# Performance work log

Hardware: AMD Instinct MI355X
Metric: run time of the kernel (lower is better)

## Reference

```python
import jax, jax.numpy as jnp
import numpy as np


def setup_inputs() -> dict:
    key = jax.random.key(0)
    k1, k2 = jax.random.split(key)
    B, Q, LD, D = 64, 32, 4096, 128
    query_embeds = jax.random.normal(k1, (B, Q, D), dtype=jnp.float32)
    doc_embeds = jax.random.normal(k2, (B, LD, D), dtype=jnp.float32)
    return {"query_embeds": query_embeds, "doc_embeds": doc_embeds}


def reference(query_embeds, doc_embeds):
    # ColBERT MaxSim (similarity_metric='maxsim'):
    # torch: (q.unsqueeze(2) * d.unsqueeze(1)).sum(-1).max(dim=-1).values.sum(-1)
    # Efficient equivalent: batched GEMM then max over doc tokens, sum over query tokens.
    # scores: [B, Q, Ld]
    scores = jnp.einsum('bqd,bld->bql', query_embeds, doc_embeds)
    # max over doc tokens (Ld), sum over query tokens (Q) -> [B]
    return jnp.max(scores, axis=-1).sum(axis=-1)
```

## Files before the change

### kernel.cpp

```cpp
#include <hip/hip_runtime.h>
#include <hip/hip_bf16.h>

typedef __attribute__((ext_vector_type(8))) short bf16x8;
typedef __attribute__((ext_vector_type(4))) float f32x4;

static constexpr int Bb = 64;
static constexpr int Qq = 32;
static constexpr int LD = 4096;
static constexpr int Dd = 128;
static constexpr int SPLITS = 8;
static constexpr int CHUNK = LD / SPLITS;
static constexpr int NWAVE = 4;
static constexpr int TPW = CHUNK / NWAVE;
static constexpr int LTILES = TPW / 16;

__device__ __forceinline__ short f2bf(float f) {
  __hip_bfloat16 h = __float2bfloat16(f);
  return *reinterpret_cast<short*>(&h);
}

__device__ __forceinline__ bf16x8 pack8(const float* __restrict__ src) {
  float4 f0 = *reinterpret_cast<const float4*>(src);
  float4 f1 = *reinterpret_cast<const float4*>(src + 4);
  bf16x8 v;
  v[0] = f2bf(f0.x); v[1] = f2bf(f0.y); v[2] = f2bf(f0.z); v[3] = f2bf(f0.w);
  v[4] = f2bf(f1.x); v[5] = f2bf(f1.y); v[6] = f2bf(f1.z); v[7] = f2bf(f1.w);
  return v;
}

__global__ __launch_bounds__(256) void maxsim_stage1(
    const float* __restrict__ qe, const float* __restrict__ de,
    float* __restrict__ pmax) {
  const int blk  = blockIdx.x;
  const int b    = blk / SPLITS;
  const int s    = blk % SPLITS;
  const int wave = threadIdx.x >> 6;
  const int lane = threadIdx.x & 63;
  const int lcol = lane & 15;
  const int lgrp = lane >> 4;

  const float* __restrict__ qb = qe + (size_t)b * Qq * Dd;
  const float* __restrict__ db = de + (size_t)b * LD * Dd;

  bf16x8 afrag[2][4];
#pragma unroll
  for (int mt = 0; mt < 2; ++mt)
#pragma unroll
    for (int kb = 0; kb < 4; ++kb)
      afrag[mt][kb] = pack8(qb + (size_t)(mt * 16 + lcol) * Dd + kb * 32 + lgrp * 8);

  float mx0[4], mx1[4];
#pragma unroll
  for (int i = 0; i < 4; ++i) { mx0[i] = -3.4e38f; mx1[i] = -3.4e38f; }

  const int tok0 = s * CHUNK + wave * TPW;
  for (int lt = 0; lt < LTILES; ++lt) {
    const float* __restrict__ trow = db + (size_t)(tok0 + lt * 16 + lcol) * Dd;
    f32x4 acc0 = {0.f, 0.f, 0.f, 0.f};
    f32x4 acc1 = {0.f, 0.f, 0.f, 0.f};
#pragma unroll
    for (int kb = 0; kb < 4; ++kb) {
      bf16x8 bfrag = pack8(trow + kb * 32 + lgrp * 8);
      acc0 = __builtin_amdgcn_mfma_f32_16x16x32_bf16(afrag[0][kb], bfrag, acc0, 0, 0, 0);
      acc1 = __builtin_amdgcn_mfma_f32_16x16x32_bf16(afrag[1][kb], bfrag, acc1, 0, 0, 0);
    }
#pragma unroll
    for (int i = 0; i < 4; ++i) {
      mx0[i] = fmaxf(mx0[i], acc0[i]);
      mx1[i] = fmaxf(mx1[i], acc1[i]);
    }
  }

#pragma unroll
  for (int off = 1; off < 16; off <<= 1) {
#pragma unroll
    for (int i = 0; i < 4; ++i) {
      mx0[i] = fmaxf(mx0[i], __shfl_xor(mx0[i], off));
      mx1[i] = fmaxf(mx1[i], __shfl_xor(mx1[i], off));
    }
  }

  __shared__ float smax[NWAVE][Qq];
  if (lcol == 0) {
#pragma unroll
    for (int i = 0; i < 4; ++i) {
      smax[wave][lgrp * 4 + i]      = mx0[i];
      smax[wave][16 + lgrp * 4 + i] = mx1[i];
    }
  }
  __syncthreads();
  if (threadIdx.x < Qq) {
    const int qi = threadIdx.x;
    float m = fmaxf(fmaxf(smax[0][qi], smax[1][qi]),
                    fmaxf(smax[2][qi], smax[3][qi]));
    pmax[((size_t)b * SPLITS + s) * Qq + qi] = m;
  }
}

__global__ __launch_bounds__(64) void maxsim_stage2(
    const float* __restrict__ pmax, float* __restrict__ out) {
  const int b = blockIdx.x;
  const int lane = threadIdx.x;
  float v = 0.f;
  if (lane < Qq) {
    float m = -3.4e38f;
#pragma unroll
    for (int s = 0; s < SPLITS; ++s)
      m = fmaxf(m, pmax[((size_t)b * SPLITS + s) * Qq + lane]);
    v = m;
  }
#pragma unroll
  for (int off = 1; off < 64; off <<= 1) v += __shfl_xor(v, off);
  if (lane == 0) out[b] = v;
}

extern "C" void kernel_launch(void* const* d_in, const int* in_sizes, int n_in,
                              void* d_out, int out_size, void* d_ws, size_t ws_size,
                              hipStream_t stream) {
  const float* qe = (const float*)d_in[0];
  const float* de = (const float*)d_in[1];
  float* out  = (float*)d_out;
  float* pmax = (float*)d_ws;

  maxsim_stage1<<<Bb * SPLITS, 256, 0, stream>>>(qe, de, pmax);
  maxsim_stage2<<<Bb, 64, 0, stream>>>(pmax, out);
}
```

Baseline: 32.01 us.

## Split query tiles across waves, double splits, and remap block order

Each wave now handles a single 16-row query tile instead of both, so the two tile waves read the same doc tokens. Splits double to 16 and blocks grow to 512 threads, with a full unroll of the token loop to put more loads in flight. Block indices are permuted so consecutive blocks land on different batch regions, which may spread traffic across XCDs. Doc data is now loaded and converted to bf16 by two waves instead of one, which doubles global reads (mostly L2 hits) and conversion work.

```diff
diff --git a/kernel.cpp b/kernel.cpp
--- a/kernel.cpp
+++ b/kernel.cpp
@@ -8,10 +8,11 @@
 static constexpr int Qq = 32;
 static constexpr int LD = 4096;
 static constexpr int Dd = 128;
-static constexpr int SPLITS = 8;
+static constexpr int SPLITS = 16;
 static constexpr int CHUNK = LD / SPLITS;
-static constexpr int NWAVE = 4;
-static constexpr int TPW = CHUNK / NWAVE;
+static constexpr int NWAVE = 8;
+static constexpr int NRANGE = NWAVE / 2;
+static constexpr int TPW = CHUNK / NRANGE;
 static constexpr int LTILES = TPW / 16;
 
 __device__ __forceinline__ short f2bf(float f) {
@@ -19,22 +20,22 @@
   return *reinterpret_cast<short*>(&h);
 }
 
-__device__ __forceinline__ bf16x8 pack8(const float* __restrict__ src) {
-  float4 f0 = *reinterpret_cast<const float4*>(src);
-  float4 f1 = *reinterpret_cast<const float4*>(src + 4);
+__device__ __forceinline__ bf16x8 cvt8(float4 a, float4 b) {
   bf16x8 v;
-  v[0] = f2bf(f0.x); v[1] = f2bf(f0.y); v[2] = f2bf(f0.z); v[3] = f2bf(f0.w);
-  v[4] = f2bf(f1.x); v[5] = f2bf(f1.y); v[6] = f2bf(f1.z); v[7] = f2bf(f1.w);
+  v[0] = f2bf(a.x); v[1] = f2bf(a.y); v[2] = f2bf(a.z); v[3] = f2bf(a.w);
+  v[4] = f2bf(b.x); v[5] = f2bf(b.y); v[6] = f2bf(b.z); v[7] = f2bf(b.w);
   return v;
 }
 
-__global__ __launch_bounds__(256) void maxsim_stage1(
+__global__ __launch_bounds__(512, 8) void maxsim_stage1(
     const float* __restrict__ qe, const float* __restrict__ de,
     float* __restrict__ pmax) {
-  const int blk  = blockIdx.x;
+  const int blk = (blockIdx.x & 7) * (Bb * SPLITS / 8) + (blockIdx.x >> 3);
   const int b    = blk / SPLITS;
   const int s    = blk % SPLITS;
   const int wave = threadIdx.x >> 6;
+  const int mt   = wave & 1;
+  const int rng  = wave >> 1;
   const int lane = threadIdx.x & 63;
   const int lcol = lane & 15;
   const int lgrp = lane >> 4;
@@ -42,57 +43,54 @@
   const float* __restrict__ qb = qe + (size_t)b * Qq * Dd;
   const float* __restrict__ db = de + (size_t)b * LD * Dd;
 
-  bf16x8 afrag[2][4];
+  bf16x8 afrag[4];
 #pragma unroll
-  for (int mt = 0; mt < 2; ++mt)
+  for (int kb = 0; kb < 4; ++kb) {
+    const float* p = qb + (size_t)(mt * 16 + lcol) * Dd + kb * 32 + lgrp * 8;
+    afrag[kb] = cvt8(*reinterpret_cast<const float4*>(p),
+                     *reinterpret_cast<const float4*>(p + 4));
+  }
+
+  float mx[4];
 #pragma unroll
-    for (int kb = 0; kb < 4; ++kb)
-      afrag[mt][kb] = pack8(qb + (size_t)(mt * 16 + lcol) * Dd + kb * 32 + lgrp * 8);
+  for (int i = 0; i < 4; ++i) mx[i] = -3.4e38f;
 
-  float mx0[4], mx1[4];
+  const int tok0 = s * CHUNK + rng * TPW;
+  const float* __restrict__ lanebase = db + (size_t)(tok0 + lcol) * Dd + lgrp * 8;
+
 #pragma unroll
-  for (int i = 0; i < 4; ++i) { mx0[i] = -3.4e38f; mx1[i] = -3.4e38f; }
-
-  const int tok0 = s * CHUNK + wave * TPW;
   for (int lt = 0; lt < LTILES; ++lt) {
-    const float* __restrict__ trow = db + (size_t)(tok0 + lt * 16 + lcol) * Dd;
-    f32x4 acc0 = {0.f, 0.f, 0.f, 0.f};
-    f32x4 acc1 = {0.f, 0.f, 0.f, 0.f};
+    const float* tb = lanebase + (size_t)lt * 16 * Dd;
+    f32x4 acc = {0.f, 0.f, 0.f, 0.f};
 #pragma unroll
     for (int kb = 0; kb < 4; ++kb) {
-      bf16x8 bfrag = pack8(trow + kb * 32 + lgrp * 8);
-      acc0 = __builtin_amdgcn_mfma_f32_16x16x32_bf16(afrag[0][kb], bfrag, acc0, 0, 0, 0);
-      acc1 = __builtin_amdgcn_mfma_f32_16x16x32_bf16(afrag[1][kb], bfrag, acc1, 0, 0, 0);
+      bf16x8 bfrag = cvt8(*reinterpret_cast<const float4*>(tb + kb * 32),
+                          *reinterpret_cast<const float4*>(tb + kb * 32 + 4));
+      acc = __builtin_amdgcn_mfma_f32_16x16x32_bf16(afrag[kb], bfrag, acc, 0, 0, 0);
     }
 #pragma unroll
-    for (int i = 0; i < 4; ++i) {
-      mx0[i] = fmaxf(mx0[i], acc0[i]);
-      mx1[i] = fmaxf(mx1[i], acc1[i]);
-    }
+    for (int i = 0; i < 4; ++i) mx[i] = fmaxf(mx[i], acc[i]);
   }
 
 #pragma unroll
-  for (int off = 1; off < 16; off <<= 1) {
+  for (int off = 1; off < 16; off <<= 1)
 #pragma unroll
-    for (int i = 0; i < 4; ++i) {
-      mx0[i] = fmaxf(mx0[i], __shfl_xor(mx0[i], off));
-      mx1[i] = fmaxf(mx1[i], __shfl_xor(mx1[i], off));
-    }
-  }
+    for (int i = 0; i < 4; ++i) mx[i] = fmaxf(mx[i], __shfl_xor(mx[i], off));
 
-  __shared__ float smax[NWAVE][Qq];
+  __shared__ float smax[NWAVE][16];
   if (lcol == 0) {
 #pragma unroll
-    for (int i = 0; i < 4; ++i) {
-      smax[wave][lgrp * 4 + i]      = mx0[i];
-      smax[wave][16 + lgrp * 4 + i] = mx1[i];
-    }
+    for (int i = 0; i < 4; ++i) smax[wave][lgrp * 4 + i] = mx[i];
   }
   __syncthreads();
   if (threadIdx.x < Qq) {
     const int qi = threadIdx.x;
-    float m = fmaxf(fmaxf(smax[0][qi], smax[1][qi]),
-                    fmaxf(smax[2][qi], smax[3][qi]));
+    const int qmt = qi >> 4;
+    const int qr  = qi & 15;
+    float m = -3.4e38f;
+#pragma unroll
+    for (int r = 0; r < NRANGE; ++r)
+      m = fmaxf(m, smax[r * 2 + qmt][qr]);
     pmax[((size_t)b * SPLITS + s) * Qq + qi] = m;
   }
 }
@@ -122,6 +120,6 @@
   float* out  = (float*)d_out;
   float* pmax = (float*)d_ws;
 
-  maxsim_stage1<<<Bb * SPLITS, 256, 0, stream>>>(qe, de, pmax);
+  maxsim_stage1<<<Bb * SPLITS, 512, 0, stream>>>(qe, de, pmax);
   maxsim_stage2<<<Bb, 64, 0, stream>>>(pmax, out);
 }
```

New measurement: 46.50 us. +45.3%, slower.
